# Kernel optimization log

Hardware: AMD Instinct MI355X
Metric: run time of the kernel (lower is better)

The kernel has to match this reference:

```python
import jax, jax.numpy as jnp
import numpy as np

EPS = 1e-6

def ln(x):
    m = jnp.mean(x, axis=-1, keepdims=True)
    v = jnp.var(x, axis=-1, keepdims=True)
    return (x - m) * jax.lax.rsqrt(v + EPS)

def modulate(x, shift, scale):
    return x * (1.0 + scale[:, None, :]) + shift[:, None, :]

def setup_inputs() -> dict:
    key = jax.random.key(0)
    ks = jax.random.split(key, 16)
    B, N, H = 2, 384, 256
    D = 128  # n_vector_features * scale_dist_features
    MIN = 2 * H + D  # 640
    FH = 1024  # swiglu_correction_fn(4.0, 256)
    s = 0.02
    inp = {
        "mask": jnp.ones((B, N), jnp.float32),
        "x": jax.random.normal(ks[0], (B, N, H), jnp.float32),
        "t_emb": jax.random.normal(ks[1], (B, H), jnp.float32),
        "dist": jax.random.normal(ks[2], (B, N, N, D), jnp.float32),
        "edge_mask": jnp.ones((B, N, N), jnp.float32),
        "W_ada": jax.random.normal(ks[3], (6 * H, H), jnp.float32) * s,
        "b_ada": jnp.zeros((6 * H,), jnp.float32),
        "W_fe1": jax.random.normal(ks[4], (H, MIN), jnp.float32) * s,
        "b_fe1": jnp.zeros((H,), jnp.float32),
        "W_fe2": jax.random.normal(ks[5], (H, H), jnp.float32) * s,
        "b_fe2": jnp.zeros((H,), jnp.float32),
        "W_qkv": jax.random.normal(ks[6], (3 * H, H), jnp.float32) * s,
        "W_out": jax.random.normal(ks[7], (H, H), jnp.float32) * s,
        "W_ffn1": jax.random.normal(ks[8], (2 * FH, H), jnp.float32) * s,
        "W_ffn2": jax.random.normal(ks[9], (H, FH), jnp.float32) * s,
    }
    return inp

def reference(mask, x, t_emb, dist, edge_mask, W_ada, b_ada, W_fe1, b_fe1,
              W_fe2, b_fe2, W_qkv, W_out, W_ffn1, W_ffn2):
    B, N, H = x.shape
    num_heads = 8
    d_head = H // num_heads
    mN = mask[..., None]  # (B,N,1)

    # adaLN modulation
    ada = jax.nn.silu(t_emb) @ W_ada.T + b_ada  # (B,6H)
    shift_msa, scale_msa, gate_msa, shift_mlp, scale_mlp, gate_mlp = jnp.split(ada, 6, axis=1)

    x_norm = modulate(ln(x * mN), shift_msa, scale_msa)  # (B,N,H)

    # all-pairs message passing: concat(h_i, h_j, dist_ij) -> MLP -> sum_j
    h1 = jnp.broadcast_to(x_norm[:, :, None, :], (B, N, N, H))
    h2 = jnp.broadcast_to(x_norm[:, None, :, :], (B, N, N, H))
    feats = jnp.concatenate([h1, h2, dist], axis=-1) * edge_mask[..., None]
    msgs = jax.nn.silu(feats @ W_fe1.T + b_fe1) @ W_fe2.T + b_fe2  # (B,N,N,H)
    x_msg = jnp.sum(msgs, axis=-2)  # (B,N,H)

    # attention
    qkv = x_msg @ W_qkv.T
    Q, K, V = jnp.split(qkv, 3, axis=-1)
    Q = ln(Q * mN)
    K = ln(K * mN)
    def heads(t):
        return t.reshape(B, N, num_heads, d_head).transpose(0, 2, 1, 3)  # b h s d
    Q, K, V = heads(Q), heads(K), heads(V)
    scores = jnp.einsum("bhqd,bhkd->bhqk", Q, K) / jnp.sqrt(jnp.float32(d_head))
    bias = jnp.where(mask[:, None, None, :] > 0, 0.0, -1e9)
    attn = jax.nn.softmax(scores + bias, axis=-1)
    ao = jnp.einsum("bhqk,bhkd->bhqd", attn, V)
    ao = ao.transpose(0, 2, 1, 3).reshape(B, N, H)
    y = ao @ W_out.T

    x = x + gate_msa[:, None, :] * y

    # SwiGLU FFN
    xm = modulate(ln(x * mN), shift_mlp, scale_mlp)
    h12 = xm @ W_ffn1.T
    h_a, h_b = jnp.split(h12, 2, axis=-1)
    ffn_out = (jax.nn.silu(h_a) * h_b) @ W_ffn2.T
    x = (x + gate_mlp[:, None, :] * ffn_out) * mN
    return x
```

## Files before the change

kernel.cpp:

```cpp
#include <hip/hip_runtime.h>

#define DEVI __device__ __forceinline__

typedef float fv4 __attribute__((ext_vector_type(4)));
typedef __bf16 bf16x8 __attribute__((ext_vector_type(8)));
typedef unsigned short u16x8 __attribute__((ext_vector_type(8)));
typedef unsigned short u16x4 __attribute__((ext_vector_type(4)));

DEVI fv4 ldv4(const float* p) { return *reinterpret_cast<const fv4*>(p); }
DEVI bf16x8 pkbf(fv4 a, fv4 b) {
  bf16x8 r;
  r[0] = (__bf16)a[0]; r[1] = (__bf16)a[1]; r[2] = (__bf16)a[2]; r[3] = (__bf16)a[3];
  r[4] = (__bf16)b[0]; r[5] = (__bf16)b[1]; r[6] = (__bf16)b[2]; r[7] = (__bf16)b[3];
  return r;
}
DEVI u16x8 b2u(bf16x8 v) { return __builtin_bit_cast(u16x8, v); }
DEVI bf16x8 asbf(u16x8 u) { return __builtin_bit_cast(bf16x8, u); }
DEVI unsigned short bfbits(float x) { __bf16 v = (__bf16)x; return __builtin_bit_cast(unsigned short, v); }
DEVI u16x4 pk4(fv4 a) {
  u16x4 u;
  u[0] = bfbits(a[0]); u[1] = bfbits(a[1]); u[2] = bfbits(a[2]); u[3] = bfbits(a[3]);
  return u;
}
DEVI fv4 MFMA16(bf16x8 a, bf16x8 b, fv4 c) {
  return __builtin_amdgcn_mfma_f32_16x16x32_bf16(a, b, c, 0, 0, 0);
}
DEVI float siluf(float x) {
  float e = __builtin_amdgcn_exp2f(x * -1.44269504f);
  return x * __builtin_amdgcn_rcpf(1.f + e);
}
DEVI fv4 glu4(fv4 x, fv4 y) {
  fv4 r;
#pragma unroll
  for (int j = 0; j < 4; ++j) r[j] = siluf(x[j]) * y[j];
  return r;
}
DEVI int swz(int row, int k) {
  int unit = k >> 3;
  int phys = (unit & ~7) | ((unit ^ row) & 7);
  return row * 384 + (phys << 3) + (k & 7);
}

__global__ __launch_bounds__(256)
void k_ada(const float* __restrict__ temb, const float* __restrict__ W_ada,
           const float* __restrict__ b_ada, float* __restrict__ ada) {
  __shared__ float sm[256];
  const int b = blockIdx.x / 6;
  const int r = (blockIdx.x % 6) * 256 + threadIdx.x;
  sm[threadIdx.x] = siluf(temb[b * 256 + threadIdx.x]);
  __syncthreads();
  float s = b_ada[r];
  const float* wr = W_ada + (size_t)r * 256;
  for (int k = 0; k < 256; ++k) s += sm[k] * wr[k];
  ada[b * 1536 + r] = s;
}

__global__ __launch_bounds__(256)
void k_xnorm(const float* __restrict__ xin, const float* __restrict__ mask,
             const float* __restrict__ ada, int shift_off, int scale_off,
             float* __restrict__ out) {
  const int row = blockIdx.x;
  const int b = row / 384;
  const int t = threadIdx.x;
  const float m = mask[row];
  const float v = xin[(size_t)row * 256 + t] * m;
  float s = v, ss = v * v;
#pragma unroll
  for (int o = 1; o < 64; o <<= 1) { s += __shfl_xor(s, o); ss += __shfl_xor(ss, o); }
  __shared__ float red[8];
  const int wid = t >> 6;
  if ((t & 63) == 0) { red[wid] = s; red[4 + wid] = ss; }
  __syncthreads();
  s = red[0] + red[1] + red[2] + red[3];
  ss = red[4] + red[5] + red[6] + red[7];
  const float mean = s * (1.f / 256.f);
  const float var = ss * (1.f / 256.f) - mean * mean;
  const float rs = rsqrtf(var + 1e-6f);
  out[(size_t)row * 256 + t] =
      (v - mean) * rs * (1.f + ada[b * 1536 + scale_off + t]) + ada[b * 1536 + shift_off + t];
}

template <int EPI, int AMODE>
__global__ __launch_bounds__(256)
void k_gemm(const float* __restrict__ A, int lda,
            const float* __restrict__ B, int ldb, int koff, int K,
            float* __restrict__ C, int ldc,
            const float* __restrict__ bias, float bscale,
            const float* __restrict__ res,
            const float* __restrict__ ada, int gate_off,
            const float* __restrict__ mask) {
  __shared__ __align__(16) unsigned short As[64 * 64];
  __shared__ __align__(16) unsigned short Bs[64 * 64];
  const int t = threadIdx.x, lane = t & 63, w = t >> 6;
  const int bn0 = blockIdx.x * 64, bm0 = blockIdx.y * 64;
  const int qr = (w >> 1) * 32, qc = (w & 1) * 32;
  const int g = lane >> 4, c = lane & 15;
  const int srow = t >> 2;
  const int so = (t & 3) * 2;
  const int o0 = so ^ (srow & 7), o1 = (so + 1) ^ (srow & 7);
  unsigned short* aw0 = As + srow * 64 + o0 * 8;
  unsigned short* aw1 = As + srow * 64 + o1 * 8;
  unsigned short* bw0 = Bs + srow * 64 + o0 * 8;
  unsigned short* bw1 = Bs + srow * 64 + o1 * 8;
  const float* ag = A + (size_t)(bm0 + srow) * lda + so * 8;
  const float* bg = B + (size_t)(bn0 + srow) * ldb + koff + so * 8;
  const float* a2g = nullptr;
  if constexpr (AMODE == 2) a2g = res + ((size_t)(bm0 + srow) * lda + so * 8);
  fv4 a0 = ldv4(ag), a1 = ldv4(ag + 4), a2 = ldv4(ag + 8), a3 = ldv4(ag + 12);
  fv4 x0, x1, x2, x3;
  if constexpr (AMODE == 1) {
    x0 = ldv4(ag + 1024); x1 = ldv4(ag + 1028); x2 = ldv4(ag + 1032); x3 = ldv4(ag + 1036);
  }
  if constexpr (AMODE == 2) {
    x0 = ldv4(a2g); x1 = ldv4(a2g + 4); x2 = ldv4(a2g + 8); x3 = ldv4(a2g + 12);
  }
  fv4 c0 = ldv4(bg), c1 = ldv4(bg + 4), c2 = ldv4(bg + 8), c3 = ldv4(bg + 12);
  fv4 acc[2][2] = {};
  for (int k0 = 0; k0 < K; k0 += 64) {
    __syncthreads();
    if constexpr (AMODE == 1) {
      *reinterpret_cast<u16x8*>(aw0) = b2u(pkbf(glu4(a0, x0), glu4(a1, x1)));
      *reinterpret_cast<u16x8*>(aw1) = b2u(pkbf(glu4(a2, x2), glu4(a3, x3)));
    } else if constexpr (AMODE == 2) {
      *reinterpret_cast<u16x8*>(aw0) = b2u(pkbf(a0 + x0, a1 + x1));
      *reinterpret_cast<u16x8*>(aw1) = b2u(pkbf(a2 + x2, a3 + x3));
    } else {
      *reinterpret_cast<u16x8*>(aw0) = b2u(pkbf(a0, a1));
      *reinterpret_cast<u16x8*>(aw1) = b2u(pkbf(a2, a3));
    }
    *reinterpret_cast<u16x8*>(bw0) = b2u(pkbf(c0, c1));
    *reinterpret_cast<u16x8*>(bw1) = b2u(pkbf(c2, c3));
    __syncthreads();
    if (k0 + 64 < K) {
      ag += 64; bg += 64;
      a0 = ldv4(ag); a1 = ldv4(ag + 4); a2 = ldv4(ag + 8); a3 = ldv4(ag + 12);
      if constexpr (AMODE == 1) {
        x0 = ldv4(ag + 1024); x1 = ldv4(ag + 1028); x2 = ldv4(ag + 1032); x3 = ldv4(ag + 1036);
      }
      if constexpr (AMODE == 2) {
        a2g += 64;
        x0 = ldv4(a2g); x1 = ldv4(a2g + 4); x2 = ldv4(a2g + 8); x3 = ldv4(a2g + 12);
      }
      c0 = ldv4(bg); c1 = ldv4(bg + 4); c2 = ldv4(bg + 8); c3 = ldv4(bg + 12);
    }
#pragma unroll
    for (int kk = 0; kk < 2; ++kk) {
      bf16x8 af[2], bf[2];
#pragma unroll
      for (int mi = 0; mi < 2; ++mi) {
        int row = qr + mi * 16 + c;
        int oct = (kk * 4 + g) ^ (row & 7);
        af[mi] = asbf(*reinterpret_cast<const u16x8*>(As + row * 64 + oct * 8));
      }
#pragma unroll
      for (int ni = 0; ni < 2; ++ni) {
        int row = qc + ni * 16 + c;
        int oct = (kk * 4 + g) ^ (row & 7);
        bf[ni] = asbf(*reinterpret_cast<const u16x8*>(Bs + row * 64 + oct * 8));
      }
#pragma unroll
      for (int mi = 0; mi < 2; ++mi)
#pragma unroll
        for (int ni = 0; ni < 2; ++ni)
          acc[mi][ni] = MFMA16(af[mi], bf[ni], acc[mi][ni]);
    }
  }
#pragma unroll
  for (int mi = 0; mi < 2; ++mi)
#pragma unroll
    for (int ni = 0; ni < 2; ++ni)
#pragma unroll
      for (int r = 0; r < 4; ++r) {
        int row = bm0 + qr + mi * 16 + g * 4 + r;
        int col = bn0 + qc + ni * 16 + c;
        float v = acc[mi][ni][r];
        if constexpr (EPI == 1) v += bscale * bias[col];
        if constexpr (EPI == 2) v = res[(size_t)row * 256 + col] + ada[(row / 384) * 1536 + gate_off + col] * v;
        if constexpr (EPI == 3) v = (res[(size_t)row * 256 + col] + ada[(row / 384) * 1536 + gate_off + col] * v) * mask[row];
        if constexpr (EPI == 5) C[(((size_t)(row >> 4) * 256 + col) << 4) + (row & 15)] = v;
        else C[(size_t)row * ldc + col] = v;
      }
}

__global__ __launch_bounds__(256)
void k_edge(const float* __restrict__ dist, const float* __restrict__ emask,
            const float* __restrict__ Wfe1, const float* __restrict__ bfe1,
            const float* __restrict__ P, const float* __restrict__ Qc,
            float* __restrict__ S0, float* __restrict__ S1) {
  const int blk = blockIdx.x, jh = blockIdx.y;
  const int b = blk / 384, i = blk - b * 384;
  const int t = threadIdx.x, lane = t & 63, w = t >> 6;
  const int g = lane >> 4, c = lane & 15;
  __shared__ __align__(16) unsigned short Al[2][16 * 128];

  bf16x8 Bf[4][4];
  float Pl[4], bl[4], Ss[4] = {0.f, 0.f, 0.f, 0.f};
#pragma unroll
  for (int ht = 0; ht < 4; ++ht) {
    const int h = w * 64 + ht * 16 + c;
    const float* wp = Wfe1 + (size_t)h * 640 + 512 + g * 8;
#pragma unroll
    for (int ks = 0; ks < 4; ++ks)
      Bf[ht][ks] = pkbf(ldv4(wp + ks * 32), ldv4(wp + ks * 32 + 4));
    Pl[ht] = P[(size_t)(b * 384 + i) * 256 + h];
    bl[ht] = bfe1[h];
  }
  const float* dbase = dist + (size_t)(b * 384 + i) * 49152 + (size_t)jh * 24576;
  const float* embase = emask + (size_t)(b * 384 + i) * 384 + jh * 192;
  const int jcb = b * 24 + jh * 12;

  const int srow = t >> 4, sunit = t & 15;
  const int sphys = (sunit & 8) | ((sunit ^ (srow & 7)) & 7);
  const int soff = srow * 128 + sphys * 8;
  const float* sg = dbase + srow * 128 + sunit * 8;

  {
    fv4 d0 = ldv4(sg), d1 = ldv4(sg + 4);
    *reinterpret_cast<u16x8*>(&Al[0][soff]) = b2u(pkbf(d0, d1));
  }
  fv4 emv = ldv4(embase + g * 4);
  fv4 qv[4];
#pragma unroll
  for (int ht = 0; ht < 4; ++ht)
    qv[ht] = ldv4(Qc + (((size_t)jcb * 256 + w * 64 + ht * 16 + c) << 4) + g * 4);
  __syncthreads();

#pragma unroll 1
  for (int cl = 0; cl < 12; ++cl) {
    fv4 p0, p1;
    if (cl < 11) {
      const float* pg = sg + (size_t)(cl + 1) * 2048;
      p0 = ldv4(pg); p1 = ldv4(pg + 4);
    }
    fv4 acc[4];
#pragma unroll
    for (int ht = 0; ht < 4; ++ht) {
#pragma unroll
      for (int r = 0; r < 4; ++r) acc[ht][r] = Pl[ht] + qv[ht][r];
    }
    const unsigned short* rb = &Al[cl & 1][0];
#pragma unroll
    for (int ks = 0; ks < 4; ++ks) {
      const int u = ks * 4 + g;
      const int phys = (u & 8) | ((u ^ (c & 7)) & 7);
      bf16x8 af = asbf(*reinterpret_cast<const u16x8*>(rb + c * 128 + phys * 8));
#pragma unroll
      for (int ht = 0; ht < 4; ++ht) acc[ht] = MFMA16(af, Bf[ht][ks], acc[ht]);
    }
    fv4 emn, qn[4];
    if (cl < 11) {
      emn = ldv4(embase + (cl + 1) * 16 + g * 4);
      const size_t jc = (size_t)(jcb + cl + 1);
#pragma unroll
      for (int ht = 0; ht < 4; ++ht)
        qn[ht] = ldv4(Qc + ((jc * 256 + w * 64 + ht * 16 + c) << 4) + g * 4);
    }
#pragma unroll
    for (int ht = 0; ht < 4; ++ht)
#pragma unroll
      for (int r = 0; r < 4; ++r)
        Ss[ht] += siluf(emv[r] * acc[ht][r] + bl[ht]);
    if (cl < 11) {
      *reinterpret_cast<u16x8*>(&Al[(cl + 1) & 1][soff]) = b2u(pkbf(p0, p1));
      emv = emn;
#pragma unroll
      for (int ht = 0; ht < 4; ++ht) qv[ht] = qn[ht];
    }
    __syncthreads();
  }
  float* Sp = jh ? S1 : S0;
#pragma unroll
  for (int ht = 0; ht < 4; ++ht) {
    float s = Ss[ht];
    s += __shfl_xor(s, 16);
    s += __shfl_xor(s, 32);
    if (g == 0) Sp[(size_t)(b * 384 + i) * 256 + w * 64 + ht * 16 + c] = s;
  }
}

__global__ __launch_bounds__(256)
void k_lnqk(const float* __restrict__ qkv, const float* __restrict__ mask,
            float* __restrict__ Qn, float* __restrict__ Kn) {
  const int row = blockIdx.x, t = threadIdx.x;
  const float m = mask[row];
  const float q = qkv[(size_t)row * 768 + t] * m;
  const float k = qkv[(size_t)row * 768 + 256 + t] * m;
  float sq = q, sqq = q * q, sk = k, skk = k * k;
#pragma unroll
  for (int o = 1; o < 64; o <<= 1) {
    sq += __shfl_xor(sq, o); sqq += __shfl_xor(sqq, o);
    sk += __shfl_xor(sk, o); skk += __shfl_xor(skk, o);
  }
  __shared__ float red[16];
  const int wid = t >> 6;
  if ((t & 63) == 0) { red[wid] = sq; red[4 + wid] = sqq; red[8 + wid] = sk; red[12 + wid] = skk; }
  __syncthreads();
  sq = red[0] + red[1] + red[2] + red[3];
  sqq = red[4] + red[5] + red[6] + red[7];
  sk = red[8] + red[9] + red[10] + red[11];
  skk = red[12] + red[13] + red[14] + red[15];
  const float mq = sq * (1.f / 256.f), vq = sqq * (1.f / 256.f) - mq * mq;
  const float mk = sk * (1.f / 256.f), vk = skk * (1.f / 256.f) - mk * mk;
  Qn[(size_t)row * 256 + t] = (q - mq) * rsqrtf(vq + 1e-6f);
  Kn[(size_t)row * 256 + t] = (k - mk) * rsqrtf(vk + 1e-6f);
}

__global__ __launch_bounds__(256)
void k_attn(const float* __restrict__ Qn, const float* __restrict__ Kn,
            const float* __restrict__ qkv, const float* __restrict__ mask,
            float* __restrict__ ao) {
  const int bh = blockIdx.y, b = bh >> 3, h = bh & 7;
  const int qg = blockIdx.x;
  const int t = threadIdx.x, lane = t & 63, w = t >> 6;
  const int g = lane >> 4, c = lane & 15;
  __shared__ __align__(16) unsigned short Vt[32 * 384];
  __shared__ __align__(16) unsigned short pl[16 * 384];
  __shared__ float outp[4][16][32];
  __shared__ float redm[4][16], reds[4][16];

  {
    const int d0 = (t & 7) * 4;
    const int kp = t >> 3;
#pragma unroll
    for (int pass = 0; pass < 6; ++pass) {
      int k = pass * 64 + kp * 2;
      fv4 v0 = ldv4(qkv + (size_t)(b * 384 + k) * 768 + 512 + h * 32 + d0);
      fv4 v1 = ldv4(qkv + (size_t)(b * 384 + k + 1) * 768 + 512 + h * 32 + d0);
#pragma unroll
      for (int j = 0; j < 4; ++j) {
        int d = d0 + j;
        unsigned int pr = (unsigned int)bfbits(v0[j]) | ((unsigned int)bfbits(v1[j]) << 16);
        *reinterpret_cast<unsigned int*>(&Vt[swz(d, k)]) = pr;
      }
    }
  }
  bf16x8 qf;
  {
    const float* qp = Qn + (size_t)(b * 384 + qg * 16 + c) * 256 + h * 32 + g * 8;
    qf = pkbf(ldv4(qp), ldv4(qp + 4));
  }
  fv4 sc[6];
#pragma unroll
  for (int kb = 0; kb < 6; ++kb) {
    const float* kp2 = Kn + (size_t)(b * 384 + w * 96 + kb * 16 + c) * 256 + h * 32 + g * 8;
    bf16x8 kf = pkbf(ldv4(kp2), ldv4(kp2 + 4));
    fv4 z = {0.f, 0.f, 0.f, 0.f};
    sc[kb] = MFMA16(qf, kf, z);
  }
  const float rs = 0.1767766952966369f;
  float zz[6][4], mx[4] = {-3e38f, -3e38f, -3e38f, -3e38f};
#pragma unroll
  for (int kb = 0; kb < 6; ++kb) {
    float mb = mask[b * 384 + w * 96 + kb * 16 + c] > 0.f ? 0.f : -1e9f;
#pragma unroll
    for (int r = 0; r < 4; ++r) {
      zz[kb][r] = sc[kb][r] * rs + mb;
      mx[r] = fmaxf(mx[r], zz[kb][r]);
    }
  }
#pragma unroll
  for (int r = 0; r < 4; ++r) {
#pragma unroll
    for (int o = 1; o < 16; o <<= 1) mx[r] = fmaxf(mx[r], __shfl_xor(mx[r], o));
  }
  if (c == 0) {
#pragma unroll
    for (int r = 0; r < 4; ++r) redm[w][g * 4 + r] = mx[r];
  }
  __syncthreads();
  float m4[4], sm[4] = {0.f, 0.f, 0.f, 0.f};
#pragma unroll
  for (int r = 0; r < 4; ++r) {
    int q = g * 4 + r;
    m4[r] = fmaxf(fmaxf(redm[0][q], redm[1][q]), fmaxf(redm[2][q], redm[3][q]));
  }
#pragma unroll
  for (int kb = 0; kb < 6; ++kb) {
    int k = w * 96 + kb * 16 + c;
#pragma unroll
    for (int r = 0; r < 4; ++r) {
      float p = __builtin_amdgcn_exp2f((zz[kb][r] - m4[r]) * 1.44269504f);
      sm[r] += p;
      pl[swz(g * 4 + r, k)] = bfbits(p);
    }
  }
#pragma unroll
  for (int r = 0; r < 4; ++r) {
#pragma unroll
    for (int o = 1; o < 16; o <<= 1) sm[r] += __shfl_xor(sm[r], o);
  }
  if (c == 0) {
#pragma unroll
    for (int r = 0; r < 4; ++r) reds[w][g * 4 + r] = sm[r];
  }
  __syncthreads();
  fv4 oacc[2] = {};
#pragma unroll
  for (int kk = 0; kk < 3; ++kk) {
    int kbase = w * 96 + kk * 32 + g * 8;
    bf16x8 pa = asbf(*reinterpret_cast<const u16x8*>(&pl[swz(c, kbase)]));
#pragma unroll
    for (int db = 0; db < 2; ++db) {
      int d = db * 16 + c;
      bf16x8 vb = asbf(*reinterpret_cast<const u16x8*>(&Vt[swz(d, kbase)]));
      oacc[db] = MFMA16(pa, vb, oacc[db]);
    }
  }
#pragma unroll
  for (int db = 0; db < 2; ++db)
#pragma unroll
    for (int r = 0; r < 4; ++r) outp[w][g * 4 + r][db * 16 + c] = oacc[db][r];
  __syncthreads();
#pragma unroll
  for (int idx = t; idx < 512; idx += 256) {
    int q = idx >> 5, d = idx & 31;
    float v = outp[0][q][d] + outp[1][q][d] + outp[2][q][d] + outp[3][q][d];
    float s = reds[0][q] + reds[1][q] + reds[2][q] + reds[3][q];
    ao[(size_t)(b * 384 + qg * 16 + q) * 256 + h * 32 + d] = v / s;
  }
}

extern "C" void kernel_launch(void* const* d_in, const int* in_sizes, int n_in,
                              void* d_out, int out_size, void* d_ws, size_t ws_size,
                              hipStream_t stream) {
  (void)in_sizes; (void)n_in; (void)out_size; (void)ws_size;
  const float* mask   = (const float*)d_in[0];
  const float* x      = (const float*)d_in[1];
  const float* temb   = (const float*)d_in[2];
  const float* dist   = (const float*)d_in[3];
  const float* emask  = (const float*)d_in[4];
  const float* W_ada  = (const float*)d_in[5];
  const float* b_ada  = (const float*)d_in[6];
  const float* W_fe1  = (const float*)d_in[7];
  const float* b_fe1  = (const float*)d_in[8];
  const float* W_fe2  = (const float*)d_in[9];
  const float* b_fe2  = (const float*)d_in[10];
  const float* W_qkv  = (const float*)d_in[11];
  const float* W_out  = (const float*)d_in[12];
  const float* W_ffn1 = (const float*)d_in[13];
  const float* W_ffn2 = (const float*)d_in[14];
  float* out = (float*)d_out;
  float* ws = (float*)d_ws;

  float* ada   = ws;
  float* xattn = ws + 4096;
  float* xm    = ws + 200704;
  float* xn    = ws + 397312;
  float* P     = ws + 593920;
  float* Qc    = ws + 790528;
  float* S0    = ws + 987136;
  float* xmsg  = ws + 1183744;
  float* qkvb  = ws + 1380352;
  float* Qn    = ws + 1970176;
  float* Kn    = ws + 2166784;
  float* aob   = ws + 2363392;
  float* S1    = ws + 2363392;
  float* h12   = ws + 397312;

  k_ada<<<12, 256, 0, stream>>>(temb, W_ada, b_ada, ada);
  k_xnorm<<<768, 256, 0, stream>>>(x, mask, ada, 0, 256, xn);
  k_gemm<0, 0><<<dim3(4, 12), 256, 0, stream>>>(xn, 256, W_fe1, 640, 0, 256, P, 256,
                                                nullptr, 0.f, nullptr, nullptr, 0, nullptr);
  k_gemm<5, 0><<<dim3(4, 12), 256, 0, stream>>>(xn, 256, W_fe1, 640, 256, 256, Qc, 0,
                                                nullptr, 0.f, nullptr, nullptr, 0, nullptr);
  k_edge<<<dim3(768, 2), 256, 0, stream>>>(dist, emask, W_fe1, b_fe1, P, Qc, S0, S1);
  k_gemm<1, 2><<<dim3(4, 12), 256, 0, stream>>>(S0, 256, W_fe2, 256, 0, 256, xmsg, 256,
                                                b_fe2, 384.f, S1, nullptr, 0, nullptr);
  k_gemm<0, 0><<<dim3(12, 12), 256, 0, stream>>>(xmsg, 256, W_qkv, 256, 0, 256, qkvb, 768,
                                                 nullptr, 0.f, nullptr, nullptr, 0, nullptr);
  k_lnqk<<<768, 256, 0, stream>>>(qkvb, mask, Qn, Kn);
  k_attn<<<dim3(24, 16), 256, 0, stream>>>(Qn, Kn, qkvb, mask, aob);
  k_gemm<2, 0><<<dim3(4, 12), 256, 0, stream>>>(aob, 256, W_out, 256, 0, 256, xattn, 256,
                                                nullptr, 0.f, x, ada, 512, nullptr);
  k_xnorm<<<768, 256, 0, stream>>>(xattn, mask, ada, 768, 1024, xm);
  k_gemm<0, 0><<<dim3(32, 12), 256, 0, stream>>>(xm, 256, W_ffn1, 256, 0, 256, h12, 2048,
                                                 nullptr, 0.f, nullptr, nullptr, 0, nullptr);
  k_gemm<3, 1><<<dim3(4, 12), 256, 0, stream>>>(h12, 2048, W_ffn2, 1024, 0, 1024, out, 256,
                                                nullptr, 0.f, xattn, ada, 1280, mask);
}
```

Before: 163.0 us.

## Stream dist and Qc tiles into LDS via async global_load_lds with 4-stage pipeline

The edge kernel now loads fp32 dist tiles and a bf16 copy of the per-j projection directly into shared memory using global_load_lds, keeping three chunks in flight in a four-buffer ring. It replaces register-staged double buffering with explicit vmcnt waits plus a barrier per iteration. The Qc projection GEMM now writes bf16 instead of fp32, halving that tensor's traffic. In exchange, the kernel uses more LDS (32KB fp32 dist plus 32KB Qc), converts to bf16 at read time, and Qc loses precision.

```diff
diff --git a/kernel.cpp b/kernel.cpp
--- a/kernel.cpp
+++ b/kernel.cpp
@@ -17,11 +17,6 @@
 DEVI u16x8 b2u(bf16x8 v) { return __builtin_bit_cast(u16x8, v); }
 DEVI bf16x8 asbf(u16x8 u) { return __builtin_bit_cast(bf16x8, u); }
 DEVI unsigned short bfbits(float x) { __bf16 v = (__bf16)x; return __builtin_bit_cast(unsigned short, v); }
-DEVI u16x4 pk4(fv4 a) {
-  u16x4 u;
-  u[0] = bfbits(a[0]); u[1] = bfbits(a[1]); u[2] = bfbits(a[2]); u[3] = bfbits(a[3]);
-  return u;
-}
 DEVI fv4 MFMA16(bf16x8 a, bf16x8 b, fv4 c) {
   return __builtin_amdgcn_mfma_f32_16x16x32_bf16(a, b, c, 0, 0, 0);
 }
@@ -34,6 +29,10 @@
 #pragma unroll
   for (int j = 0; j < 4; ++j) r[j] = siluf(x[j]) * y[j];
   return r;
+}
+DEVI void gld16(const float* g, const void* l) {
+  __builtin_amdgcn_global_load_lds((const __attribute__((address_space(1))) void*)g,
+                                   (__attribute__((address_space(3))) void*)l, 16, 0, 0);
 }
 DEVI int swz(int row, int k) {
   int unit = k >> 3;
@@ -174,24 +173,29 @@
         int row = bm0 + qr + mi * 16 + g * 4 + r;
         int col = bn0 + qc + ni * 16 + c;
         float v = acc[mi][ni][r];
-        if constexpr (EPI == 1) v += bscale * bias[col];
-        if constexpr (EPI == 2) v = res[(size_t)row * 256 + col] + ada[(row / 384) * 1536 + gate_off + col] * v;
-        if constexpr (EPI == 3) v = (res[(size_t)row * 256 + col] + ada[(row / 384) * 1536 + gate_off + col] * v) * mask[row];
-        if constexpr (EPI == 5) C[(((size_t)(row >> 4) * 256 + col) << 4) + (row & 15)] = v;
-        else C[(size_t)row * ldc + col] = v;
+        if constexpr (EPI == 6) {
+          ((unsigned short*)C)[(((size_t)(row >> 4) * 256 + col) << 4) + (row & 15)] = bfbits(v);
+        } else {
+          if constexpr (EPI == 1) v += bscale * bias[col];
+          if constexpr (EPI == 2) v = res[(size_t)row * 256 + col] + ada[(row / 384) * 1536 + gate_off + col] * v;
+          if constexpr (EPI == 3) v = (res[(size_t)row * 256 + col] + ada[(row / 384) * 1536 + gate_off + col] * v) * mask[row];
+          C[(size_t)row * ldc + col] = v;
+        }
       }
 }
 
 __global__ __launch_bounds__(256)
 void k_edge(const float* __restrict__ dist, const float* __restrict__ emask,
             const float* __restrict__ Wfe1, const float* __restrict__ bfe1,
-            const float* __restrict__ P, const float* __restrict__ Qc,
+            const float* __restrict__ P, const unsigned short* __restrict__ Qb,
             float* __restrict__ S0, float* __restrict__ S1) {
   const int blk = blockIdx.x, jh = blockIdx.y;
   const int b = blk / 384, i = blk - b * 384;
   const int t = threadIdx.x, lane = t & 63, w = t >> 6;
   const int g = lane >> 4, c = lane & 15;
-  __shared__ __align__(16) unsigned short Al[2][16 * 128];
+  __shared__ __align__(16) float Dl[4][16 * 128];
+  __shared__ __align__(16) unsigned short Ql[4][256 * 16];
+  __shared__ __align__(16) float eml[192];
 
   bf16x8 Bf[4][4];
   float Pl[4], bl[4], Ss[4] = {0.f, 0.f, 0.f, 0.f};
@@ -206,67 +210,71 @@
     bl[ht] = bfe1[h];
   }
   const float* dbase = dist + (size_t)(b * 384 + i) * 49152 + (size_t)jh * 24576;
-  const float* embase = emask + (size_t)(b * 384 + i) * 384 + jh * 192;
-  const int jcb = b * 24 + jh * 12;
-
-  const int srow = t >> 4, sunit = t & 15;
-  const int sphys = (sunit & 8) | ((sunit ^ (srow & 7)) & 7);
-  const int soff = srow * 128 + sphys * 8;
-  const float* sg = dbase + srow * 128 + sunit * 8;
-
-  {
-    fv4 d0 = ldv4(sg), d1 = ldv4(sg + 4);
-    *reinterpret_cast<u16x8*>(&Al[0][soff]) = b2u(pkbf(d0, d1));
-  }
-  fv4 emv = ldv4(embase + g * 4);
-  fv4 qv[4];
-#pragma unroll
-  for (int ht = 0; ht < 4; ++ht)
-    qv[ht] = ldv4(Qc + (((size_t)jcb * 256 + w * 64 + ht * 16 + c) << 4) + g * 4);
+  const unsigned short* qbase = Qb + (size_t)(b * 24 + jh * 12) * 4096;
+  if (t < 192) eml[t] = emask[(size_t)(b * 384 + i) * 384 + jh * 192 + t];
+
+  int doff[2];
+#pragma unroll
+  for (int k = 0; k < 2; ++k) {
+    int r = w * 4 + k * 2 + (lane >> 5);
+    int p = lane & 31;
+    int u = (p & ~7) | ((p ^ (r & 7)) & 7);
+    doff[k] = r * 128 + u * 4;
+  }
+#pragma unroll
+  for (int ch = 0; ch < 3; ++ch) {
+#pragma unroll
+    for (int k = 0; k < 2; ++k) {
+      gld16(dbase + ch * 2048 + doff[k], &Dl[ch][w * 512 + k * 256]);
+      gld16((const float*)(qbase + ch * 4096 + w * 1024 + k * 512 + lane * 8),
+            &Ql[ch][w * 1024 + k * 512]);
+    }
+  }
   __syncthreads();
 
 #pragma unroll 1
   for (int cl = 0; cl < 12; ++cl) {
-    fv4 p0, p1;
-    if (cl < 11) {
-      const float* pg = sg + (size_t)(cl + 1) * 2048;
-      p0 = ldv4(pg); p1 = ldv4(pg + 4);
-    }
+    if (cl < 10)       asm volatile("s_waitcnt vmcnt(8)" ::: "memory");
+    else if (cl == 10) asm volatile("s_waitcnt vmcnt(4)" ::: "memory");
+    else               asm volatile("s_waitcnt vmcnt(0)" ::: "memory");
+    __builtin_amdgcn_s_barrier();
+    __builtin_amdgcn_sched_barrier(0);
+    if (cl < 9) {
+      const int ch = cl + 3, bi2 = ch & 3;
+#pragma unroll
+      for (int k = 0; k < 2; ++k) {
+        gld16(dbase + (size_t)ch * 2048 + doff[k], &Dl[bi2][w * 512 + k * 256]);
+        gld16((const float*)(qbase + (size_t)ch * 4096 + w * 1024 + k * 512 + lane * 8),
+              &Ql[bi2][w * 1024 + k * 512]);
+      }
+    }
+    const int bi = cl & 3;
+    fv4 emv = *reinterpret_cast<const fv4*>(&eml[cl * 16 + g * 4]);
     fv4 acc[4];
 #pragma unroll
     for (int ht = 0; ht < 4; ++ht) {
-#pragma unroll
-      for (int r = 0; r < 4; ++r) acc[ht][r] = Pl[ht] + qv[ht][r];
-    }
-    const unsigned short* rb = &Al[cl & 1][0];
+      const int h = w * 64 + ht * 16 + c;
+      u16x4 qb4 = *reinterpret_cast<const u16x4*>(&Ql[bi][h * 16 + g * 4]);
+#pragma unroll
+      for (int r = 0; r < 4; ++r)
+        acc[ht][r] = Pl[ht] + __builtin_bit_cast(float, ((unsigned)qb4[r]) << 16);
+    }
 #pragma unroll
     for (int ks = 0; ks < 4; ++ks) {
-      const int u = ks * 4 + g;
-      const int phys = (u & 8) | ((u ^ (c & 7)) & 7);
-      bf16x8 af = asbf(*reinterpret_cast<const u16x8*>(rb + c * 128 + phys * 8));
+      const int u0 = ks * 8 + g * 2;
+      const int ph0 = (u0 & ~7) | ((u0 ^ (c & 7)) & 7);
+      const int ph1 = ((u0 + 1) & ~7) | (((u0 + 1) ^ (c & 7)) & 7);
+      fv4 d0 = *reinterpret_cast<const fv4*>(&Dl[bi][c * 128 + ph0 * 4]);
+      fv4 d1 = *reinterpret_cast<const fv4*>(&Dl[bi][c * 128 + ph1 * 4]);
+      bf16x8 af = pkbf(d0, d1);
 #pragma unroll
       for (int ht = 0; ht < 4; ++ht) acc[ht] = MFMA16(af, Bf[ht][ks], acc[ht]);
-    }
-    fv4 emn, qn[4];
-    if (cl < 11) {
-      emn = ldv4(embase + (cl + 1) * 16 + g * 4);
-      const size_t jc = (size_t)(jcb + cl + 1);
-#pragma unroll
-      for (int ht = 0; ht < 4; ++ht)
-        qn[ht] = ldv4(Qc + ((jc * 256 + w * 64 + ht * 16 + c) << 4) + g * 4);
     }
 #pragma unroll
     for (int ht = 0; ht < 4; ++ht)
 #pragma unroll
       for (int r = 0; r < 4; ++r)
         Ss[ht] += siluf(emv[r] * acc[ht][r] + bl[ht]);
-    if (cl < 11) {
-      *reinterpret_cast<u16x8*>(&Al[(cl + 1) & 1][soff]) = b2u(pkbf(p0, p1));
-      emv = emn;
-#pragma unroll
-      for (int ht = 0; ht < 4; ++ht) qv[ht] = qn[ht];
-    }
-    __syncthreads();
   }
   float* Sp = jh ? S1 : S0;
 #pragma unroll
@@ -317,7 +325,6 @@
   __shared__ __align__(16) unsigned short pl[16 * 384];
   __shared__ float outp[4][16][32];
   __shared__ float redm[4][16], reds[4][16];
-
   {
     const int d0 = (t & 7) * 4;
     const int kp = t >> 3;
@@ -461,9 +468,10 @@
   k_xnorm<<<768, 256, 0, stream>>>(x, mask, ada, 0, 256, xn);
   k_gemm<0, 0><<<dim3(4, 12), 256, 0, stream>>>(xn, 256, W_fe1, 640, 0, 256, P, 256,
                                                 nullptr, 0.f, nullptr, nullptr, 0, nullptr);
-  k_gemm<5, 0><<<dim3(4, 12), 256, 0, stream>>>(xn, 256, W_fe1, 640, 256, 256, Qc, 0,
+  k_gemm<6, 0><<<dim3(4, 12), 256, 0, stream>>>(xn, 256, W_fe1, 640, 256, 256, Qc, 0,
                                                 nullptr, 0.f, nullptr, nullptr, 0, nullptr);
-  k_edge<<<dim3(768, 2), 256, 0, stream>>>(dist, emask, W_fe1, b_fe1, P, Qc, S0, S1);
+  k_edge<<<dim3(768, 2), 256, 0, stream>>>(dist, emask, W_fe1, b_fe1, P,
+                                           (const unsigned short*)Qc, S0, S1);
   k_gemm<1, 2><<<dim3(4, 12), 256, 0, stream>>>(S0, 256, W_fe2, 256, 0, 256, xmsg, 256,
                                                 b_fe2, 384.f, S1, nullptr, 0, nullptr);
   k_gemm<0, 0><<<dim3(12, 12), 256, 0, stream>>>(xmsg, 256, W_qkv, 256, 0, 256, qkvb, 768,
```

New measurement: 162.2 us. No clear change (-0.5%).
